# Optimization experiments

Hardware: AMD Instinct MI355X
Metric: run time of the kernel (lower is better)

The kernel has to match this reference:

```python
import jax, jax.numpy as jnp
import numpy as np

DIM = 1024
E = 8
TOP_K = 2
HID = int(DIM * 2.68)  # 2744


def setup_inputs() -> dict:
    key = jax.random.key(0)
    ks = jax.random.split(key, 8)
    s = 0.02
    return {
        "x": jax.random.normal(ks[0], (4, 1024, DIM), dtype=jnp.float32),
        "gate_w": jax.random.normal(ks[1], (E, DIM), dtype=jnp.float32) * s,
        "w1": jax.random.normal(ks[2], (E, HID, DIM), dtype=jnp.float32) * s,
        "w2": jax.random.normal(ks[3], (E, HID, DIM), dtype=jnp.float32) * s,
        "w3": jax.random.normal(ks[4], (E, DIM, HID), dtype=jnp.float32) * s,
        "sw1": jax.random.normal(ks[5], (HID, DIM), dtype=jnp.float32) * s,
        "sw2": jax.random.normal(ks[6], (HID, DIM), dtype=jnp.float32) * s,
        "sw3": jax.random.normal(ks[7], (DIM, HID), dtype=jnp.float32) * s,
    }


def reference(x, gate_w, w1, w2, w3, sw1, sw2, sw3):
    B, T, C = x.shape
    xf = x.reshape(-1, C)  # [S, C]
    logits = xf @ gate_w.T  # [S, E]
    rw = jax.nn.softmax(logits.astype(jnp.float32), axis=-1)
    tkw, tki = jax.lax.top_k(rw, TOP_K)  # [S, K]
    nE = rw.shape[-1]
    importance = rw.mean(0)  # [E]
    load = jax.nn.one_hot(tki[:, 0], nE, dtype=jnp.float32).mean(0)  # [E]
    aux_loss = nE * (importance * load).sum()
    tkw = tkw / tkw.sum(-1, keepdims=True)
    tkw = tkw.astype(x.dtype)
    # dense all-expert SwiGLU (faithful to original: every expert on every token)
    h = jax.nn.silu(jnp.einsum('sc,ehc->seh', xf, w1)) * jnp.einsum('sc,ehc->seh', xf, w2)  # [S,E,H]
    eo = jnp.einsum('seh,ech->sec', h, w3)  # [S, E, C]
    sel = jnp.take_along_axis(eo, tki[:, :, None], axis=1)  # [S, K, C]
    weighted = (sel * tkw[:, :, None]).sum(1)  # [S, C]
    shared = (jax.nn.silu(xf @ sw1.T) * (xf @ sw2.T)) @ sw3.T  # [S, C]
    y = (weighted + shared).reshape(B, T, C)
    return y, aux_loss
```

## Files before the change

### kernel.cpp

```cpp
#include <hip/hip_runtime.h>
#include <cstdio>
#include <cstdint>

#define S_TOK 4096
#define CDIM  1024
#define EXP   8
#define HRAW  2744
#define HPAD  2816
#define MAXROWS  13312
#define MAXTILES 104
#define NSLICE1  (HPAD / 128)
#define NSLICE2  (CDIM / 256)
#define G1_BLKS  (MAXTILES * NSLICE1)

typedef __attribute__((ext_vector_type(8))) short bf16x8;
typedef __attribute__((ext_vector_type(4))) float f32x4;
typedef __attribute__((ext_vector_type(4))) unsigned short us4;
typedef unsigned short us;

__device__ __forceinline__ us f2bf(float f) {
  unsigned u = __float_as_uint(f);
  u += 0x7fffu + ((u >> 16) & 1u);
  return (us)(u >> 16);
}

__device__ __forceinline__ void gl16(const us* g, us* l) {
  __builtin_amdgcn_global_load_lds((__attribute__((address_space(1))) void*)g,
                                   (__attribute__((address_space(3))) void*)l,
                                   16, 0, 0);
}

__device__ __forceinline__ int xcd_swz(int orig, int nwg) {
  int q = nwg >> 3, r = nwg & 7;
  int x = orig & 7, idx = orig >> 3;
  return (x < r ? x * (q + 1) : r * (q + 1) + (x - r) * q) + idx;
}

#define CH_RP1  (HPAD * CDIM / 4)
#define CH_CPR  (HPAD / 4)

__device__ __forceinline__ void cvt4_rowpad(const float* __restrict__ src,
                                            us* __restrict__ dst, int idx) {
  int m = idx / CH_RP1, rem = idx - m * CH_RP1;
  int r = rem >> 8, c4 = rem & 255;
  us4 o;
  if (r < HRAW) {
    float4 v = *(const float4*)(src + ((size_t)(m * HRAW + r) * CDIM + c4 * 4));
    o.x = f2bf(v.x); o.y = f2bf(v.y); o.z = f2bf(v.z); o.w = f2bf(v.w);
  } else { o.x = 0; o.y = 0; o.z = 0; o.w = 0; }
  *(us4*)(dst + ((size_t)(m * HPAD + r) * CDIM + c4 * 4)) = o;
}

__device__ __forceinline__ void cvt4_colpad(const float* __restrict__ src,
                                            us* __restrict__ dst, int idx) {
  int r = idx / CH_CPR, c4 = idx - r * CH_CPR;
  int c = c4 * 4;
  us4 o;
  if (c < HRAW) {
    float4 v = *(const float4*)(src + (size_t)r * HRAW + c);
    o.x = f2bf(v.x); o.y = f2bf(v.y); o.z = f2bf(v.z); o.w = f2bf(v.w);
  } else { o.x = 0; o.y = 0; o.z = 0; o.w = 0; }
  *(us4*)(dst + (size_t)r * HPAD + c) = o;
}

__global__ void __launch_bounds__(256) gate_kernel(const float* __restrict__ x,
                                                   const float* __restrict__ gw,
                                                   us* __restrict__ xb,
                                                   int* __restrict__ tki,
                                                   float* __restrict__ tkw,
                                                   float* __restrict__ probs) {
  const int wv = threadIdx.x >> 6, lane = threadIdx.x & 63;
  const int s = blockIdx.x * 4 + wv;
  const float4* xs4 = (const float4*)(x + (size_t)s * CDIM);
  float acc[8] = {0, 0, 0, 0, 0, 0, 0, 0};
#pragma unroll
  for (int j = 0; j < 4; j++) {
    float4 v = xs4[lane * 4 + j];
    int c = lane * 16 + j * 4;
    us4 ov;
    ov.x = f2bf(v.x); ov.y = f2bf(v.y); ov.z = f2bf(v.z); ov.w = f2bf(v.w);
    *(us4*)(xb + (size_t)s * CDIM + c) = ov;
#pragma unroll
    for (int ee = 0; ee < 8; ee++) {
      const float* g = gw + ee * CDIM + c;
      acc[ee] += v.x * g[0] + v.y * g[1] + v.z * g[2] + v.w * g[3];
    }
  }
#pragma unroll
  for (int ee = 0; ee < 8; ee++) {
#pragma unroll
    for (int off = 32; off > 0; off >>= 1) acc[ee] += __shfl_xor(acc[ee], off, 64);
  }
  if (lane == 0) {
    float mx = acc[0];
    for (int ee = 1; ee < 8; ee++) mx = fmaxf(mx, acc[ee]);
    float p[8], sm = 0.f;
    for (int ee = 0; ee < 8; ee++) { p[ee] = expf(acc[ee] - mx); sm += p[ee]; }
    float inv = 1.f / sm;
    for (int ee = 0; ee < 8; ee++) probs[s * 8 + ee] = p[ee] * inv;
    int i0 = 0; float b0 = p[0];
    for (int ee = 1; ee < 8; ee++) if (p[ee] > b0) { b0 = p[ee]; i0 = ee; }
    int i1 = -1; float b1 = -1.f;
    for (int ee = 0; ee < 8; ee++) if (ee != i0 && p[ee] > b1) { b1 = p[ee]; i1 = ee; }
    float rw0 = b0 * inv, rw1 = b1 * inv;
    float den = 1.f / (rw0 + rw1);
    tki[2 * s] = i0; tki[2 * s + 1] = i1;
    tkw[2 * s] = rw0 * den; tkw[2 * s + 1] = rw1 * den;
  }
}

#define CVTAB_BLKS 2048
#define AB_W1   (8 * CH_RP1)
#define AB_W2   (AB_W1 + 8 * CH_RP1)
#define AB_SW1  (AB_W2 + CH_RP1)
#define AB_SW2  (AB_SW1 + CH_RP1)

__global__ void __launch_bounds__(512) cvtab_build_kernel(
    const float* __restrict__ w1, const float* __restrict__ w2,
    const float* __restrict__ sw1, const float* __restrict__ sw2,
    us* __restrict__ w1b, us* __restrict__ w2b,
    us* __restrict__ sw1b, us* __restrict__ sw2b,
    const int* __restrict__ tki, const float* __restrict__ tkw,
    const float* __restrict__ probs, int* __restrict__ meta,
    int* __restrict__ pairtok, float* __restrict__ pairw,
    int* __restrict__ invmap, int* __restrict__ tile_expert,
    float* __restrict__ aux_out) {
  if (blockIdx.x == 0) {
    const int tid = threadIdx.x, lane = tid & 63, wv = tid >> 6;
    __shared__ int s_cnt[EXP];
    __shared__ int s_amc[EXP];
    __shared__ float s_imp[EXP];
    {
      const int e = wv;
      int c_cnt = 0, c_amc = 0;
      float imp = 0.f;
      for (int s0 = 0; s0 < S_TOK; s0 += 64) {
        int s = s0 + lane;
        int i0 = tki[2 * s], i1 = tki[2 * s + 1];
        c_cnt += (i0 == e) || (i1 == e);
        c_amc += (i0 == e);
        imp += probs[s * 8 + e];
      }
#pragma unroll
      for (int off = 32; off > 0; off >>= 1) {
        c_cnt += __shfl_xor(c_cnt, off, 64);
        c_amc += __shfl_xor(c_amc, off, 64);
        imp   += __shfl_xor(imp, off, 64);
      }
      if (lane == 0) { s_cnt[e] = c_cnt; s_amc[e] = c_amc; s_imp[e] = imp; }
    }
    __syncthreads();
    int pad[EXP], start[EXP];
    int o = S_TOK;
#pragma unroll
    for (int j = 0; j < EXP; j++) {
      pad[j] = ((s_cnt[j] + 127) >> 7) << 7;
      start[j] = o;
      o += pad[j];
    }
    const int total = o;
    for (int r = tid; r < S_TOK; r += 512) { pairtok[r] = r; pairw[r] = 1.f; }
    {
      const int e = wv;
      int base = start[e];
      for (int s0 = 0; s0 < S_TOK; s0 += 64) {
        int s = s0 + lane;
        int i0 = tki[2 * s], i1 = tki[2 * s + 1];
        bool m0 = (i0 == e), m1 = (i1 == e);
        bool mm = m0 || m1;
        unsigned long long mk = __ballot(mm);
        if (mm) {
          int pos = base + __popcll(mk & ((1ull << lane) - 1ull));
          pairtok[pos] = s;
          pairw[pos] = m0 ? tkw[2 * s] : tkw[2 * s + 1];
          invmap[2 * s + (m0 ? 0 : 1)] = pos;
        }
        base += __popcll(mk);
      }
      for (int r = base + lane; r < start[e] + pad[e]; r += 64) {
        pairtok[r] = -1; pairw[r] = 0.f;
      }
    }
    if (tid < 128) {
      int ex = 8;
      if (tid >= 32) {
        int rr = tid * 128;
#pragma unroll
        for (int j = 0; j < EXP; j++)
          if (rr >= start[j] && rr < start[j] + pad[j]) ex = j;
      }
      tile_expert[tid] = ex;
    }
    if (tid == 0) {
      meta[0] = total >> 7;
      float a = 0.f;
      for (int j = 0; j < EXP; j++)
        a += (s_imp[j] * (1.f / 4096.f)) * ((float)s_amc[j] * (1.f / 4096.f));
      aux_out[0] = 8.f * a;
    }
    return;
  }
  for (int i = (blockIdx.x - 1) * 512 + threadIdx.x; i < AB_SW2;
       i += (CVTAB_BLKS - 1) * 512) {
    if (i < AB_W1)       cvt4_rowpad(w1,  w1b,  i);
    else if (i < AB_W2)  cvt4_rowpad(w2,  w2b,  i - AB_W1);
    else if (i < AB_SW1) cvt4_rowpad(sw1, sw1b, i - AB_W2);
    else                 cvt4_rowpad(sw2, sw2b, i - AB_SW1);
  }
}

#define W3CVT_BLKS 1024
#define W3_CHUNKS  (8 * CDIM * CH_CPR)
#define W3TOT      (W3_CHUNKS + CDIM * CH_CPR)

__global__ void __launch_bounds__(256, 2) gemm1_kernel(
    const us* __restrict__ xb, const us* __restrict__ w1b, const us* __restrict__ w2b,
    const us* __restrict__ sw1b, const us* __restrict__ sw2b,
    const int* __restrict__ pairtok, const int* __restrict__ tile_expert,
    const int* __restrict__ meta, us* __restrict__ h,
    const float* __restrict__ w3, const float* __restrict__ sw3,
    us* __restrict__ w3b, us* __restrict__ sw3b) {
  if (blockIdx.x >= G1_BLKS) {
    for (int i = (blockIdx.x - G1_BLKS) * 256 + threadIdx.x; i < W3TOT;
         i += W3CVT_BLKS * 256) {
      if (i < W3_CHUNKS) cvt4_colpad(w3,  w3b,  i);
      else               cvt4_colpad(sw3, sw3b, i - W3_CHUNKS);
    }
    return;
  }
  const int wgid = xcd_swz(blockIdx.x, G1_BLKS);
  const int mt = wgid % MAXTILES;
  if (mt >= meta[0]) return;
  const int n0 = (wgid / MAXTILES) * 128;
  const int e = tile_expert[mt];
  const us* B1 = (e == 8) ? sw1b : (w1b + (size_t)e * HPAD * CDIM);
  const us* B2 = (e == 8) ? sw2b : (w2b + (size_t)e * HPAD * CDIM);
  const int row0 = mt * 128;
  __shared__ __align__(16) us sA[128 * 32];
  __shared__ __align__(16) us sB1[128 * 32];
  __shared__ __align__(16) us sB2[128 * 32];
  const int tid = threadIdx.x, lane = tid & 63;
  const int wm = tid >> 7, wn = (tid >> 6) & 1;
  const int sub = tid & 3, ra = tid >> 2;
  const int subx = sub ^ ((ra >> 1) & 3);
  int t0 = pairtok[row0 + ra];      if (t0 < 0) t0 = 0;
  int t1 = pairtok[row0 + 64 + ra]; if (t1 < 0) t1 = 0;
  const us* gA0 = xb + (size_t)t0 * CDIM + subx * 8;
  const us* gA1 = xb + (size_t)t1 * CDIM + subx * 8;
  const us* gB1a = B1 + (size_t)(n0 + ra) * CDIM + subx * 8;
  const us* gB1b = B1 + (size_t)(n0 + 64 + ra) * CDIM + subx * 8;
  const us* gB2a = B2 + (size_t)(n0 + ra) * CDIM + subx * 8;
  const us* gB2b = B2 + (size_t)(n0 + 64 + ra) * CDIM + subx * 8;
  f32x4 au[4][4], av[4][4];
#pragma unroll
  for (int m = 0; m < 4; m++)
#pragma unroll
    for (int n = 0; n < 4; n++)
#pragma unroll
      for (int r = 0; r < 4; r++) { au[m][n][r] = 0.f; av[m][n][r] = 0.f; }

  const int rl = lane & 15;
  const int kx = (((lane >> 4) ^ ((lane >> 1) & 3)) << 3);
  for (int k0 = 0; k0 < CDIM; k0 += 32) {
    gl16(gA0 + k0,  &sA[tid * 8]);
    gl16(gA1 + k0,  &sA[(tid + 256) * 8]);
    gl16(gB1a + k0, &sB1[tid * 8]);
    gl16(gB1b + k0, &sB1[(tid + 256) * 8]);
    gl16(gB2a + k0, &sB2[tid * 8]);
    gl16(gB2b + k0, &sB2[(tid + 256) * 8]);
    __syncthreads();
    bf16x8 a[4], b1[4], b2[4];
#pragma unroll
    for (int m = 0; m < 4; m++)
      a[m] = *(const bf16x8*)&sA[(wm * 64 + m * 16 + rl) * 32 + kx];
#pragma unroll
    for (int n = 0; n < 4; n++) {
      b1[n] = *(const bf16x8*)&sB1[(wn * 64 + n * 16 + rl) * 32 + kx];
      b2[n] = *(const bf16x8*)&sB2[(wn * 64 + n * 16 + rl) * 32 + kx];
    }
#pragma unroll
    for (int m = 0; m < 4; m++)
#pragma unroll
      for (int n = 0; n < 4; n++) {
        au[m][n] = __builtin_amdgcn_mfma_f32_16x16x32_bf16(a[m], b1[n], au[m][n], 0, 0, 0);
        av[m][n] = __builtin_amdgcn_mfma_f32_16x16x32_bf16(a[m], b2[n], av[m][n], 0, 0, 0);
      }
    __syncthreads();
  }
  const int rb = (lane >> 4) * 4, cb = lane & 15;
#pragma unroll
  for (int m = 0; m < 4; m++)
#pragma unroll
    for (int n = 0; n < 4; n++)
#pragma unroll
      for (int r = 0; r < 4; r++) {
        int row = row0 + wm * 64 + m * 16 + rb + r;
        int col = n0 + wn * 64 + n * 16 + cb;
        float u = au[m][n][r], v = av[m][n][r];
        float sg = 1.f / (1.f + __expf(-u));
        h[(size_t)row * HPAD + col] = f2bf(u * sg * v);
      }
}

__global__ void __launch_bounds__(256, 2) gemm2_kernel(
    const us* __restrict__ h, const us* __restrict__ w3b, const us* __restrict__ sw3b,
    const int* __restrict__ tile_expert, const int* __restrict__ meta,
    float* __restrict__ eo) {
  const int wgid = xcd_swz(blockIdx.x, MAXTILES * NSLICE2);
  const int mt = wgid % MAXTILES;
  if (mt >= meta[0]) return;
  const int n0 = (wgid / MAXTILES) * 256;
  const int e = tile_expert[mt];
  const us* B = (e == 8) ? sw3b : (w3b + (size_t)e * CDIM * HPAD);
  const int row0 = mt * 128;
  __shared__ __align__(16) us sA[128 * 32];
  __shared__ __align__(16) us sB[256 * 32];
  const int tid = threadIdx.x, lane = tid & 63;
  const int wm = tid >> 7, wn = (tid >> 6) & 1;
  const int sub = tid & 3, ra = tid >> 2;
  const int subx = sub ^ ((ra >> 1) & 3);
  const us* gA0 = h + (size_t)(row0 + ra) * HPAD + subx * 8;
  const us* gA1 = h + (size_t)(row0 + 64 + ra) * HPAD + subx * 8;
  const us* gB0 = B + (size_t)(n0 + ra) * HPAD + subx * 8;
  const us* gB1 = B + (size_t)(n0 + 64 + ra) * HPAD + subx * 8;
  const us* gB2 = B + (size_t)(n0 + 128 + ra) * HPAD + subx * 8;
  const us* gB3 = B + (size_t)(n0 + 192 + ra) * HPAD + subx * 8;
  f32x4 ac[4][8];
#pragma unroll
  for (int m = 0; m < 4; m++)
#pragma unroll
    for (int n = 0; n < 8; n++)
#pragma unroll
      for (int r = 0; r < 4; r++) ac[m][n][r] = 0.f;

  const int rl = lane & 15;
  const int kx = (((lane >> 4) ^ ((lane >> 1) & 3)) << 3);
  for (int k0 = 0; k0 < HPAD; k0 += 32) {
    gl16(gA0 + k0, &sA[tid * 8]);
    gl16(gA1 + k0, &sA[(tid + 256) * 8]);
    gl16(gB0 + k0, &sB[tid * 8]);
    gl16(gB1 + k0, &sB[(tid + 256) * 8]);
    gl16(gB2 + k0, &sB[(tid + 512) * 8]);
    gl16(gB3 + k0, &sB[(tid + 768) * 8]);
    __syncthreads();
    bf16x8 a[4], b[8];
#pragma unroll
    for (int m = 0; m < 4; m++)
      a[m] = *(const bf16x8*)&sA[(wm * 64 + m * 16 + rl) * 32 + kx];
#pragma unroll
    for (int n = 0; n < 8; n++)
      b[n] = *(const bf16x8*)&sB[(wn * 128 + n * 16 + rl) * 32 + kx];
#pragma unroll
    for (int m = 0; m < 4; m++)
#pragma unroll
      for (int n = 0; n < 8; n++)
        ac[m][n] = __builtin_amdgcn_mfma_f32_16x16x32_bf16(a[m], b[n], ac[m][n], 0, 0, 0);
    __syncthreads();
  }
  const int rb = (lane >> 4) * 4, cb = lane & 15;
#pragma unroll
  for (int m = 0; m < 4; m++)
#pragma unroll
    for (int n = 0; n < 8; n++)
#pragma unroll
      for (int r = 0; r < 4; r++) {
        int row = row0 + wm * 64 + m * 16 + rb + r;
        int col = n0 + wn * 128 + n * 16 + cb;
        eo[(size_t)row * CDIM + col] = ac[m][n][r];
      }
}

__global__ void __launch_bounds__(256) combine_kernel(const float* __restrict__ eo,
                                                      const int* __restrict__ invmap,
                                                      const float* __restrict__ pairw,
                                                      float* __restrict__ out) {
  const int s = blockIdx.x;
  const int c = threadIdx.x * 4;
  const int j0 = invmap[2 * s], j1 = invmap[2 * s + 1];
  const float w0 = pairw[j0], w1 = pairw[j1];
  float4 a = *(const float4*)(eo + (size_t)s * CDIM + c);
  float4 b = *(const float4*)(eo + (size_t)j0 * CDIM + c);
  float4 d = *(const float4*)(eo + (size_t)j1 * CDIM + c);
  float4 o;
  o.x = a.x + w0 * b.x + w1 * d.x;
  o.y = a.y + w0 * b.y + w1 * d.y;
  o.z = a.z + w0 * b.z + w1 * d.z;
  o.w = a.w + w0 * b.w + w1 * d.w;
  *(float4*)(out + (size_t)s * CDIM + c) = o;
}

extern "C" void kernel_launch(void* const* d_in, const int* in_sizes, int n_in,
                              void* d_out, int out_size, void* d_ws, size_t ws_size,
                              hipStream_t stream) {
  const float* x   = (const float*)d_in[0];
  const float* gw  = (const float*)d_in[1];
  const float* w1  = (const float*)d_in[2];
  const float* w2  = (const float*)d_in[3];
  const float* w3  = (const float*)d_in[4];
  const float* sw1 = (const float*)d_in[5];
  const float* sw2 = (const float*)d_in[6];
  const float* sw3 = (const float*)d_in[7];
  float* out = (float*)d_out;
  char* ws = (char*)d_ws;
  size_t off = 0;
  auto take = [&](size_t bytes) -> char* {
    char* p = ws + off;
    off = (off + bytes + 255) & ~(size_t)255;
    return p;
  };
  us* xb    = (us*)take((size_t)S_TOK * CDIM * 2);
  us* w1b   = (us*)take((size_t)EXP * HPAD * CDIM * 2);
  us* w2b   = (us*)take((size_t)EXP * HPAD * CDIM * 2);
  us* w3b   = (us*)take((size_t)EXP * CDIM * HPAD * 2);
  us* sw1b  = (us*)take((size_t)HPAD * CDIM * 2);
  us* sw2b  = (us*)take((size_t)HPAD * CDIM * 2);
  us* sw3b  = (us*)take((size_t)CDIM * HPAD * 2);
  us* hbuf  = (us*)take((size_t)MAXROWS * HPAD * 2);
  int* pairtok = (int*)take(MAXROWS * 4);
  float* pairw = (float*)take(MAXROWS * 4);
  int* invmap  = (int*)take(S_TOK * 2 * 4);
  int* tile_expert = (int*)take(128 * 4);
  int* tki = (int*)take(S_TOK * 2 * 4);
  float* tkw = (float*)take(S_TOK * 2 * 4);
  float* probs = (float*)take(S_TOK * EXP * 4);
  int* meta = (int*)take(256);
  float* eo = (float*)w1b;
  if (off > ws_size) {
    fprintf(stderr, "MoE kernel: ws too small, need %zu got %zu\n", off, ws_size);
    return;
  }
  gate_kernel<<<S_TOK / 4, 256, 0, stream>>>(x, gw, xb, tki, tkw, probs);
  cvtab_build_kernel<<<CVTAB_BLKS, 512, 0, stream>>>(
      w1, w2, sw1, sw2, w1b, w2b, sw1b, sw2b,
      tki, tkw, probs, meta, pairtok, pairw, invmap, tile_expert,
      out + (size_t)S_TOK * CDIM);
  gemm1_kernel<<<G1_BLKS + W3CVT_BLKS, 256, 0, stream>>>(
      xb, w1b, w2b, sw1b, sw2b, pairtok, tile_expert, meta, hbuf,
      w3, sw3, w3b, sw3b);
  gemm2_kernel<<<MAXTILES * NSLICE2, 256, 0, stream>>>(
      hbuf, w3b, sw3b, tile_expert, meta, eo);
  combine_kernel<<<S_TOK, 256, 0, stream>>>(eo, invmap, pairw, out);
}
```

Before: 429.4 us.

## Double GEMM K-step to 64 with 8-way LDS swizzle; store expert outputs as bf16

Both grouped GEMM kernels now load a 64-wide K slice per iteration instead of 32. Each row splits into eight 16-byte octets, and the LDS layout is XOR-swizzled on the row index. This halves the number of barriers and loop iterations per output tile, at the cost of twice the LDS footprint, which may limit occupancy. The expert-output buffer is also stored in bf16 rather than fp32 and moved into its own workspace region, halving gemm2 store traffic and combine read traffic in exchange for extra rounding before the weighted sum.

New measurement: 400.8 us. 6.7% less time.

```diff
diff --git a/kernel.cpp b/kernel.cpp
--- a/kernel.cpp
+++ b/kernel.cpp
@@ -22,6 +22,9 @@
   unsigned u = __float_as_uint(f);
   u += 0x7fffu + ((u >> 16) & 1u);
   return (us)(u >> 16);
+}
+__device__ __forceinline__ float bf2f(us v) {
+  return __uint_as_float((unsigned)v << 16);
 }
 
 __device__ __forceinline__ void gl16(const us* g, us* l) {
@@ -236,21 +239,23 @@
   const us* B1 = (e == 8) ? sw1b : (w1b + (size_t)e * HPAD * CDIM);
   const us* B2 = (e == 8) ? sw2b : (w2b + (size_t)e * HPAD * CDIM);
   const int row0 = mt * 128;
-  __shared__ __align__(16) us sA[128 * 32];
-  __shared__ __align__(16) us sB1[128 * 32];
-  __shared__ __align__(16) us sB2[128 * 32];
+  __shared__ __align__(16) us sA[128 * 64];
+  __shared__ __align__(16) us sB1[128 * 64];
+  __shared__ __align__(16) us sB2[128 * 64];
   const int tid = threadIdx.x, lane = tid & 63;
   const int wm = tid >> 7, wn = (tid >> 6) & 1;
-  const int sub = tid & 3, ra = tid >> 2;
-  const int subx = sub ^ ((ra >> 1) & 3);
-  int t0 = pairtok[row0 + ra];      if (t0 < 0) t0 = 0;
-  int t1 = pairtok[row0 + 64 + ra]; if (t1 < 0) t1 = 0;
-  const us* gA0 = xb + (size_t)t0 * CDIM + subx * 8;
-  const us* gA1 = xb + (size_t)t1 * CDIM + subx * 8;
-  const us* gB1a = B1 + (size_t)(n0 + ra) * CDIM + subx * 8;
-  const us* gB1b = B1 + (size_t)(n0 + 64 + ra) * CDIM + subx * 8;
-  const us* gB2a = B2 + (size_t)(n0 + ra) * CDIM + subx * 8;
-  const us* gB2b = B2 + (size_t)(n0 + 64 + ra) * CDIM + subx * 8;
+  const int srow = tid >> 3;
+  const int soct = (tid & 7) ^ (srow & 7);
+  const us* gA[4];
+  const us* gB1a[4];
+  const us* gB2a[4];
+#pragma unroll
+  for (int j = 0; j < 4; j++) {
+    int t = pairtok[row0 + j * 32 + srow]; if (t < 0) t = 0;
+    gA[j]   = xb + (size_t)t * CDIM + soct * 8;
+    gB1a[j] = B1 + (size_t)(n0 + j * 32 + srow) * CDIM + soct * 8;
+    gB2a[j] = B2 + (size_t)(n0 + j * 32 + srow) * CDIM + soct * 8;
+  }
   f32x4 au[4][4], av[4][4];
 #pragma unroll
   for (int m = 0; m < 4; m++)
@@ -259,32 +264,37 @@
 #pragma unroll
       for (int r = 0; r < 4; r++) { au[m][n][r] = 0.f; av[m][n][r] = 0.f; }
 
-  const int rl = lane & 15;
-  const int kx = (((lane >> 4) ^ ((lane >> 1) & 3)) << 3);
-  for (int k0 = 0; k0 < CDIM; k0 += 32) {
-    gl16(gA0 + k0,  &sA[tid * 8]);
-    gl16(gA1 + k0,  &sA[(tid + 256) * 8]);
-    gl16(gB1a + k0, &sB1[tid * 8]);
-    gl16(gB1b + k0, &sB1[(tid + 256) * 8]);
-    gl16(gB2a + k0, &sB2[tid * 8]);
-    gl16(gB2b + k0, &sB2[(tid + 256) * 8]);
+  const int rl = lane & 15, fo = lane >> 4;
+  const int x0 = ((0 + fo) ^ (rl & 7)) << 3;
+  const int x1 = ((4 + fo) ^ (rl & 7)) << 3;
+  for (int k0 = 0; k0 < CDIM; k0 += 64) {
+#pragma unroll
+    for (int j = 0; j < 4; j++) {
+      gl16(gA[j] + k0,   &sA[(j * 256 + tid) * 8]);
+      gl16(gB1a[j] + k0, &sB1[(j * 256 + tid) * 8]);
+      gl16(gB2a[j] + k0, &sB2[(j * 256 + tid) * 8]);
+    }
     __syncthreads();
-    bf16x8 a[4], b1[4], b2[4];
-#pragma unroll
-    for (int m = 0; m < 4; m++)
-      a[m] = *(const bf16x8*)&sA[(wm * 64 + m * 16 + rl) * 32 + kx];
-#pragma unroll
-    for (int n = 0; n < 4; n++) {
-      b1[n] = *(const bf16x8*)&sB1[(wn * 64 + n * 16 + rl) * 32 + kx];
-      b2[n] = *(const bf16x8*)&sB2[(wn * 64 + n * 16 + rl) * 32 + kx];
-    }
-#pragma unroll
-    for (int m = 0; m < 4; m++)
+#pragma unroll
+    for (int ks = 0; ks < 2; ks++) {
+      const int kx = ks ? x1 : x0;
+      bf16x8 a[4], b1[4], b2[4];
+#pragma unroll
+      for (int m = 0; m < 4; m++)
+        a[m] = *(const bf16x8*)&sA[(wm * 64 + m * 16 + rl) * 64 + kx];
 #pragma unroll
       for (int n = 0; n < 4; n++) {
-        au[m][n] = __builtin_amdgcn_mfma_f32_16x16x32_bf16(a[m], b1[n], au[m][n], 0, 0, 0);
-        av[m][n] = __builtin_amdgcn_mfma_f32_16x16x32_bf16(a[m], b2[n], av[m][n], 0, 0, 0);
-      }
+        b1[n] = *(const bf16x8*)&sB1[(wn * 64 + n * 16 + rl) * 64 + kx];
+        b2[n] = *(const bf16x8*)&sB2[(wn * 64 + n * 16 + rl) * 64 + kx];
+      }
+#pragma unroll
+      for (int m = 0; m < 4; m++)
+#pragma unroll
+        for (int n = 0; n < 4; n++) {
+          au[m][n] = __builtin_amdgcn_mfma_f32_16x16x32_bf16(a[m], b1[n], au[m][n], 0, 0, 0);
+          av[m][n] = __builtin_amdgcn_mfma_f32_16x16x32_bf16(a[m], b2[n], av[m][n], 0, 0, 0);
+        }
+    }
     __syncthreads();
   }
   const int rb = (lane >> 4) * 4, cb = lane & 15;
@@ -305,7 +315,7 @@
 __global__ void __launch_bounds__(256, 2) gemm2_kernel(
     const us* __restrict__ h, const us* __restrict__ w3b, const us* __restrict__ sw3b,
     const int* __restrict__ tile_expert, const int* __restrict__ meta,
-    float* __restrict__ eo) {
+    us* __restrict__ eo) {
   const int wgid = xcd_swz(blockIdx.x, MAXTILES * NSLICE2);
   const int mt = wgid % MAXTILES;
   if (mt >= meta[0]) return;
@@ -313,18 +323,20 @@
   const int e = tile_expert[mt];
   const us* B = (e == 8) ? sw3b : (w3b + (size_t)e * CDIM * HPAD);
   const int row0 = mt * 128;
-  __shared__ __align__(16) us sA[128 * 32];
-  __shared__ __align__(16) us sB[256 * 32];
+  __shared__ __align__(16) us sA[128 * 64];
+  __shared__ __align__(16) us sB[256 * 64];
   const int tid = threadIdx.x, lane = tid & 63;
   const int wm = tid >> 7, wn = (tid >> 6) & 1;
-  const int sub = tid & 3, ra = tid >> 2;
-  const int subx = sub ^ ((ra >> 1) & 3);
-  const us* gA0 = h + (size_t)(row0 + ra) * HPAD + subx * 8;
-  const us* gA1 = h + (size_t)(row0 + 64 + ra) * HPAD + subx * 8;
-  const us* gB0 = B + (size_t)(n0 + ra) * HPAD + subx * 8;
-  const us* gB1 = B + (size_t)(n0 + 64 + ra) * HPAD + subx * 8;
-  const us* gB2 = B + (size_t)(n0 + 128 + ra) * HPAD + subx * 8;
-  const us* gB3 = B + (size_t)(n0 + 192 + ra) * HPAD + subx * 8;
+  const int srow = tid >> 3;
+  const int soct = (tid & 7) ^ (srow & 7);
+  const us* gA[4];
+  const us* gB[8];
+#pragma unroll
+  for (int j = 0; j < 4; j++)
+    gA[j] = h + (size_t)(row0 + j * 32 + srow) * HPAD + soct * 8;
+#pragma unroll
+  for (int j = 0; j < 8; j++)
+    gB[j] = B + (size_t)(n0 + j * 32 + srow) * HPAD + soct * 8;
   f32x4 ac[4][8];
 #pragma unroll
   for (int m = 0; m < 4; m++)
@@ -333,28 +345,33 @@
 #pragma unroll
       for (int r = 0; r < 4; r++) ac[m][n][r] = 0.f;
 
-  const int rl = lane & 15;
-  const int kx = (((lane >> 4) ^ ((lane >> 1) & 3)) << 3);
-  for (int k0 = 0; k0 < HPAD; k0 += 32) {
-    gl16(gA0 + k0, &sA[tid * 8]);
-    gl16(gA1 + k0, &sA[(tid + 256) * 8]);
-    gl16(gB0 + k0, &sB[tid * 8]);
-    gl16(gB1 + k0, &sB[(tid + 256) * 8]);
-    gl16(gB2 + k0, &sB[(tid + 512) * 8]);
-    gl16(gB3 + k0, &sB[(tid + 768) * 8]);
+  const int rl = lane & 15, fo = lane >> 4;
+  const int x0 = ((0 + fo) ^ (rl & 7)) << 3;
+  const int x1 = ((4 + fo) ^ (rl & 7)) << 3;
+  for (int k0 = 0; k0 < HPAD; k0 += 64) {
+#pragma unroll
+    for (int j = 0; j < 4; j++)
+      gl16(gA[j] + k0, &sA[(j * 256 + tid) * 8]);
+#pragma unroll
+    for (int j = 0; j < 8; j++)
+      gl16(gB[j] + k0, &sB[(j * 256 + tid) * 8]);
     __syncthreads();
-    bf16x8 a[4], b[8];
-#pragma unroll
-    for (int m = 0; m < 4; m++)
-      a[m] = *(const bf16x8*)&sA[(wm * 64 + m * 16 + rl) * 32 + kx];
-#pragma unroll
-    for (int n = 0; n < 8; n++)
-      b[n] = *(const bf16x8*)&sB[(wn * 128 + n * 16 + rl) * 32 + kx];
-#pragma unroll
-    for (int m = 0; m < 4; m++)
+#pragma unroll
+    for (int ks = 0; ks < 2; ks++) {
+      const int kx = ks ? x1 : x0;
+      bf16x8 a[4], b[8];
+#pragma unroll
+      for (int m = 0; m < 4; m++)
+        a[m] = *(const bf16x8*)&sA[(wm * 64 + m * 16 + rl) * 64 + kx];
 #pragma unroll
       for (int n = 0; n < 8; n++)
-        ac[m][n] = __builtin_amdgcn_mfma_f32_16x16x32_bf16(a[m], b[n], ac[m][n], 0, 0, 0);
+        b[n] = *(const bf16x8*)&sB[(wn * 128 + n * 16 + rl) * 64 + kx];
+#pragma unroll
+      for (int m = 0; m < 4; m++)
+#pragma unroll
+        for (int n = 0; n < 8; n++)
+          ac[m][n] = __builtin_amdgcn_mfma_f32_16x16x32_bf16(a[m], b[n], ac[m][n], 0, 0, 0);
+    }
     __syncthreads();
   }
   const int rb = (lane >> 4) * 4, cb = lane & 15;
@@ -366,11 +383,11 @@
       for (int r = 0; r < 4; r++) {
         int row = row0 + wm * 64 + m * 16 + rb + r;
         int col = n0 + wn * 128 + n * 16 + cb;
-        eo[(size_t)row * CDIM + col] = ac[m][n][r];
-      }
-}
-
-__global__ void __launch_bounds__(256) combine_kernel(const float* __restrict__ eo,
+        eo[(size_t)row * CDIM + col] = f2bf(ac[m][n][r]);
+      }
+}
+
+__global__ void __launch_bounds__(256) combine_kernel(const us* __restrict__ eo,
                                                       const int* __restrict__ invmap,
                                                       const float* __restrict__ pairw,
                                                       float* __restrict__ out) {
@@ -378,14 +395,14 @@
   const int c = threadIdx.x * 4;
   const int j0 = invmap[2 * s], j1 = invmap[2 * s + 1];
   const float w0 = pairw[j0], w1 = pairw[j1];
-  float4 a = *(const float4*)(eo + (size_t)s * CDIM + c);
-  float4 b = *(const float4*)(eo + (size_t)j0 * CDIM + c);
-  float4 d = *(const float4*)(eo + (size_t)j1 * CDIM + c);
+  us4 a = *(const us4*)(eo + (size_t)s * CDIM + c);
+  us4 b = *(const us4*)(eo + (size_t)j0 * CDIM + c);
+  us4 d = *(const us4*)(eo + (size_t)j1 * CDIM + c);
   float4 o;
-  o.x = a.x + w0 * b.x + w1 * d.x;
-  o.y = a.y + w0 * b.y + w1 * d.y;
-  o.z = a.z + w0 * b.z + w1 * d.z;
-  o.w = a.w + w0 * b.w + w1 * d.w;
+  o.x = bf2f(a.x) + w0 * bf2f(b.x) + w1 * bf2f(d.x);
+  o.y = bf2f(a.y) + w0 * bf2f(b.y) + w1 * bf2f(d.y);
+  o.z = bf2f(a.z) + w0 * bf2f(b.z) + w1 * bf2f(d.z);
+  o.w = bf2f(a.w) + w0 * bf2f(b.w) + w1 * bf2f(d.w);
   *(float4*)(out + (size_t)s * CDIM + c) = o;
 }
 
@@ -416,6 +433,7 @@
   us* sw2b  = (us*)take((size_t)HPAD * CDIM * 2);
   us* sw3b  = (us*)take((size_t)CDIM * HPAD * 2);
   us* hbuf  = (us*)take((size_t)MAXROWS * HPAD * 2);
+  us* eo    = (us*)take((size_t)MAXROWS * CDIM * 2);
   int* pairtok = (int*)take(MAXROWS * 4);
   float* pairw = (float*)take(MAXROWS * 4);
   int* invmap  = (int*)take(S_TOK * 2 * 4);
@@ -424,7 +442,6 @@
   float* tkw = (float*)take(S_TOK * 2 * 4);
   float* probs = (float*)take(S_TOK * EXP * 4);
   int* meta = (int*)take(256);
-  float* eo = (float*)w1b;
   if (off > ws_size) {
     fprintf(stderr, "MoE kernel: ws too small, need %zu got %zu\n", off, ws_size);
     return;
```
